# Kernel tuning notes

Measured on AMD Instinct MI355X. Metric: run time of the kernel, lower is better.

The kernel has to match this reference:

```python
import jax, jax.numpy as jnp
import numpy as np

D = 1024      # d_model
H = 16        # n_heads
HD = D // H   # head_dim = 64
B = 2
T = 2048


def setup_inputs() -> dict:
    key = jax.random.key(0)
    k0, k1, k2 = jax.random.split(key, 3)
    s = 1.0 / np.sqrt(D)
    return {
        "x": jax.random.normal(k0, (B, T, D), dtype=jnp.float32),
        "qkv_w": jax.random.normal(k1, (D, 3 * D), dtype=jnp.float32) * s,
        "qkv_b": jnp.zeros((3 * D,), dtype=jnp.float32),
        "out_w": jax.random.normal(k2, (D, D), dtype=jnp.float32) * s,
        "out_b": jnp.zeros((D,), dtype=jnp.float32),
    }


def _apply_rotary(x, rope):
    # Faithful to the torch apply_rotary: even/odd interleaved split of both
    # x and the [sin(freqs)|cos(freqs)] rope table.
    x1, x2 = x[..., ::2], x[..., 1::2]
    sin, cos = rope[..., ::2], rope[..., 1::2]
    return jnp.concatenate([x1 * cos - x2 * sin, x1 * sin + x2 * cos], axis=-1)


def reference(x, qkv_w, qkv_b, out_w, out_b):
    Bx, Tx, Dm = x.shape
    # QKV projection -> [3, B, H, T, HD]
    qkv = (x @ qkv_w + qkv_b).reshape(Bx, Tx, 3, H, HD).transpose(2, 0, 3, 1, 4)
    q, k, v = qkv[0], qkv[1], qkv[2]

    # Rotary table: rope = concat(sin(freqs), cos(freqs)) along last dim -> [T, HD]
    inv_freq = 1.0 / (10000.0 ** (jnp.arange(0, HD, 2, dtype=jnp.float32) / HD))
    t = jnp.arange(Tx, dtype=jnp.float32)
    freqs = t[:, None] * inv_freq[None, :]          # [T, HD/2]
    rope = jnp.concatenate([jnp.sin(freqs), jnp.cos(freqs)], axis=-1)  # [T, HD]

    q = _apply_rotary(q, rope)
    k = _apply_rotary(k, rope)

    scale = HD ** -0.5
    scores = jnp.einsum('bhqd,bhkd->bhqk', q, k) * scale  # [B,H,T,T]
    causal_mask = jnp.triu(jnp.ones((Tx, Tx), dtype=bool), 1)
    scores = jnp.where(causal_mask, -jnp.inf, scores)
    attn = jax.nn.softmax(scores, axis=-1)
    # dropout is identity in eval mode
    out = jnp.einsum('bhqk,bhkd->bhqd', attn, v)           # [B,H,T,HD]
    out = out.transpose(0, 2, 1, 3).reshape(Bx, Tx, Dm)    # [B,T,D]
    return out @ out_w + out_b
```

## Files before the change

### kernel.cpp

```cpp
#include <hip/hip_runtime.h>

typedef unsigned short u16;
typedef __attribute__((ext_vector_type(8))) __bf16 bf16x8;
typedef __attribute__((ext_vector_type(4))) float f32x4;

#define NB 2
#define NT 2048
#define ND 1024
#define NH 16
#define HD 64

__device__ __forceinline__ float b2f(u16 u) {
  union { float f; unsigned int i; } v; v.i = ((unsigned int)u) << 16; return v.f;
}
__device__ __forceinline__ u16 f2b(float f) {
  union { float f; unsigned int i; } v; v.f = f;
  unsigned int r = (v.i + 0x7FFFu + ((v.i >> 16) & 1u)) >> 16;
  return (u16)r;
}
__device__ __forceinline__ unsigned int cvtpk(float lo, float hi) {
  unsigned int pk;
  asm("v_cvt_pk_bf16_f32 %0, %1, %2" : "=v"(pk) : "v"(lo), "v"(hi));
  return pk;
}

__device__ __forceinline__ void gload_lds16(const u16* g, u16* lds) {
  __builtin_amdgcn_global_load_lds(
      (const __attribute__((address_space(1))) unsigned int*)(g),
      (__attribute__((address_space(3))) unsigned int*)(lds),
      16, 0, 0);
}

__device__ __forceinline__ f32x4 mfma16(bf16x8 a, bf16x8 b, f32x4 c) {
  return __builtin_amdgcn_mfma_f32_16x16x32_bf16(a, b, c, 0, 0, 0);
}

template <int N>
__device__ __forceinline__ float ror16(float x) {
  return __int_as_float(__builtin_amdgcn_update_dpp(
      __float_as_int(x), __float_as_int(x), 0x120 | N, 0xF, 0xF, true));
}
__device__ __forceinline__ float rsum16(float x) {
  x += ror16<8>(x);
  x += ror16<4>(x);
  x += ror16<2>(x);
  x += ror16<1>(x);
  return x;
}

__device__ __forceinline__ float fast_sin(float a) {
  float r = a * 0.15915494309189535f;
  r -= floorf(r);
  return __builtin_amdgcn_sinf(r);
}
__device__ __forceinline__ float fast_cos(float a) {
  float r = a * 0.15915494309189535f;
  r -= floorf(r);
  return __builtin_amdgcn_cosf(r);
}

__global__ __launch_bounds__(256) void prep_inputs(
    const float* __restrict__ x, const float* __restrict__ qkv_w,
    const float* __restrict__ out_w, u16* __restrict__ xb,
    u16* __restrict__ wqkvT, u16* __restrict__ woutT) {
  __shared__ u16 tile[32][33];
  const int blk = blockIdx.x;
  const int tid = threadIdx.x;
  if (blk < 2048) {
    int i = (blk * 256 + tid) * 8;
#pragma unroll
    for (int j = 0; j < 8; ++j) xb[i + j] = f2b(x[i + j]);
    return;
  }
  const float* in; u16* out; int N; int idx;
  if (blk < 5120) { idx = blk - 2048; in = qkv_w; out = wqkvT; N = 3072; }
  else            { idx = blk - 5120; in = out_w; out = woutT; N = 1024; }
  const int nbx = N / 32;
  const int n0 = (idx % nbx) * 32, k0 = (idx / nbx) * 32;
  const int tx = tid & 31, ty = tid >> 5;
  for (int i2 = ty; i2 < 32; i2 += 8)
    tile[i2][tx] = f2b(in[(size_t)(k0 + i2) * N + n0 + tx]);
  __syncthreads();
  for (int i2 = ty; i2 < 32; i2 += 8)
    out[(size_t)(n0 + i2) * 1024 + k0 + tx] = tile[tx][i2];
}

__global__ __launch_bounds__(256, 2) void gemm128_2ph(const u16* __restrict__ A,
                                                      const u16* __restrict__ Bt,
                                                      const float* __restrict__ bias,
                                                      float* __restrict__ C,
                                                      int M, int N, int K) {
  __shared__ alignas(16) u16 lds[2][2][8192];
  const int tid = threadIdx.x;
  const int lane = tid & 63;
  const int wave = tid >> 6;
  const int l15 = lane & 15, quad = lane >> 4;
  const int wm = (wave >> 1) * 64, wn = (wave & 1) * 64;

  const int lin = blockIdx.y * gridDim.x + blockIdx.x;
  const int xcd = lin & 7, loc = lin >> 3;
  const int row0 = (xcd * 4 + (loc >> 3)) * 128;
  const int col0 = (loc & 7) * 128;

  const int sr = tid >> 3;
  const size_t soff = (size_t)sr * K + (size_t)((tid & 7) ^ (sr & 7)) * 8;
  const u16* Ab = A + (size_t)row0 * K;
  const u16* Bb = Bt + (size_t)col0 * K;

  const int swz0 = (quad ^ (l15 & 7)) * 8;
  const int swz1 = ((4 + quad) ^ (l15 & 7)) * 8;
  const int arow = (wm + l15) * 64;
  const int brow = (wn + l15) * 64;

  f32x4 acc[4][4] = {};
  const int NTIL = K >> 6;

#define STAGE8(dst, bptr, koff)                                              \
  _Pragma("unroll") for (int p = 0; p < 4; ++p)                              \
      gload_lds16((bptr) + (koff) + soff + (size_t)p * 32 * K,               \
                  &(dst)[(p * 256 + tid) * 8]);

  STAGE8(lds[0][0], Ab, 0);
  STAGE8(lds[0][1], Bb, 0);
  asm volatile("s_waitcnt vmcnt(0)");
  __builtin_amdgcn_s_barrier();
  asm volatile("" ::: "memory");

  for (int t = 0; t < NTIL; ++t) {
    const int cur = t & 1;
    if (t + 1 < NTIL) {
      STAGE8(lds[cur ^ 1][0], Ab, (size_t)(t + 1) * 64);
      STAGE8(lds[cur ^ 1][1], Bb, (size_t)(t + 1) * 64);
    }
    bf16x8 af[4][2], bfr[4][2];
#pragma unroll
    for (int i = 0; i < 4; ++i) {
      af[i][0]  = *(const bf16x8*)&lds[cur][0][arow + i * 1024 + swz0];
      af[i][1]  = *(const bf16x8*)&lds[cur][0][arow + i * 1024 + swz1];
      bfr[i][0] = *(const bf16x8*)&lds[cur][1][brow + i * 1024 + swz0];
      bfr[i][1] = *(const bf16x8*)&lds[cur][1][brow + i * 1024 + swz1];
    }
    asm volatile("s_waitcnt lgkmcnt(0)");
    __builtin_amdgcn_sched_barrier(0);
#pragma unroll
    for (int i = 0; i < 4; ++i)
#pragma unroll
      for (int j = 0; j < 4; ++j) {
        acc[i][j] = mfma16(af[i][0], bfr[j][0], acc[i][j]);
        acc[i][j] = mfma16(af[i][1], bfr[j][1], acc[i][j]);
      }
    asm volatile("s_waitcnt vmcnt(0)");
    __builtin_amdgcn_s_barrier();
    asm volatile("" ::: "memory");
  }
#undef STAGE8

#pragma unroll
  for (int j = 0; j < 4; ++j) {
    const int c = col0 + wn + j * 16 + l15;
    const float bv = bias[c];
#pragma unroll
    for (int i = 0; i < 4; ++i) {
      const int rr0 = row0 + wm + i * 16 + quad * 4;
      f32x4 v = acc[i][j];
#pragma unroll
      for (int rr = 0; rr < 4; ++rr)
        C[(size_t)(rr0 + rr) * N + c] = v[rr] + bv;
    }
  }
}

__device__ __forceinline__ void stage2(const u16* g0, const u16* g1, u16* l,
                                       int tid) {
  gload_lds16(g0, &l[tid * 8]);
  gload_lds16(g1, &l[(512 + tid) * 8]);
}

#define AH(b, h) (&lds[((b) * 2 + (h)) * 8192])
#define BH(b, h) (&lds[32768 + ((b) * 2 + (h)) * 8192])

#define LOAD_AFX(dst, base)                                                 \
  _Pragma("unroll") for (int mm = 0; mm < 4; ++mm) {                        \
    dst[mm][0] = *(const bf16x8*)&(base)[arow + mm * 2048 + swz0];          \
    dst[mm][1] = *(const bf16x8*)&(base)[arow + mm * 2048 + swz1];          \
  }
#define LOAD_BF(base)                                                       \
  _Pragma("unroll") for (int nn = 0; nn < 2; ++nn) {                        \
    bfr[nn][0] = *(const bf16x8*)&(base)[brow + nn * 4096 + swz0];          \
    bfr[nn][1] = *(const bf16x8*)&(base)[brow + nn * 4096 + swz1];          \
  }
#define MFMA_QX(afv, MA, NQ)                                                \
  _Pragma("unroll") for (int mm = 0; mm < 4; ++mm)                          \
  _Pragma("unroll") for (int nn = 0; nn < 2; ++nn) {                        \
    acc[(MA) * 4 + mm][(NQ) * 2 + nn] =                                     \
        mfma16(afv[mm][0], bfr[nn][0], acc[(MA) * 4 + mm][(NQ) * 2 + nn]);  \
    acc[(MA) * 4 + mm][(NQ) * 2 + nn] =                                     \
        mfma16(afv[mm][1], bfr[nn][1], acc[(MA) * 4 + mm][(NQ) * 2 + nn]);  \
  }
#define PH_SYNC                                                             \
  __builtin_amdgcn_s_barrier();                                             \
  asm volatile("s_waitcnt lgkmcnt(0)");                                     \
  __builtin_amdgcn_sched_barrier(0);                                        \
  __builtin_amdgcn_s_setprio(1);
#define PH_END                                                              \
  __builtin_amdgcn_s_setprio(0);                                            \
  __builtin_amdgcn_s_barrier();                                             \
  asm volatile("" ::: "memory");

__global__ __launch_bounds__(512, 2) void gemm256_bt(const u16* __restrict__ A,
                                                     const u16* __restrict__ Bt,
                                                     const float* __restrict__ bias,
                                                     u16* __restrict__ C,
                                                     int M, int N, int K) {
  __shared__ alignas(16) u16 lds[65536];
  const int tid = threadIdx.x;
  const int lane = tid & 63;
  const int wave = tid >> 6;
  const int l15 = lane & 15, quad = lane >> 4;
  const int wm = wave >> 2, wn = wave & 3;

  const int lin = blockIdx.y * gridDim.x + blockIdx.x;
  const int xcd = lin & 7, loc = lin >> 3;
  const int row0 = ((xcd & 3) * 4 + loc / 6) * 256;
  const int col0 = ((xcd >> 2) * 6 + loc % 6) * 256;
  const int NTIL = K >> 6;

  const int sr = tid >> 3;
  const size_t soff = (size_t)sr * K + (size_t)((tid & 7) ^ (sr & 7)) * 8;
  const size_t hK = (size_t)64 * K;
  const u16* A0p = A + (size_t)row0 * K + soff;
  const u16* A1p = A0p + 2 * hK;
  const u16* B0p = Bt + (size_t)col0 * K + soff;
  const u16* B1p = B0p + 2 * hK;

  const int swz0 = (quad ^ (l15 & 7)) * 8;
  const int swz1 = ((4 + quad) ^ (l15 & 7)) * 8;
  const int arow = (wm * 16 + l15) * 64;
  const int brow = (wn * 16 + l15) * 64;

  f32x4 acc[8][4] = {};

  stage2(B0p, B0p + hK, BH(0, 0), tid);
  stage2(A1p, A1p + hK, AH(0, 1), tid);
  stage2(A0p, A0p + hK, AH(0, 0), tid);
  stage2(B1p, B1p + hK, BH(0, 1), tid);
  {
    int tp = (NTIL > 1) ? 1 : 0;
    stage2(B0p + tp * 64, B0p + tp * 64 + hK, BH(1, 0), tid);
    stage2(A1p + tp * 64, A1p + tp * 64 + hK, AH(1, 1), tid);
  }
  asm volatile("s_waitcnt vmcnt(4)");
  __builtin_amdgcn_s_barrier();
  asm volatile("" ::: "memory");

  bf16x8 afA[4][2], afB[4][2], bfr[2][2];
#pragma unroll 2
  for (int t = 0; t < NTIL; ++t) {
    const int cur = t & 1, nxt = cur ^ 1;
    const int o1 = ((t + 1 < NTIL) ? t + 1 : NTIL - 1) * 64;
    const int o2 = ((t + 2 < NTIL) ? t + 2 : NTIL - 1) * 64;
    u16* Ac0 = AH(cur, 0);
    u16* Ac1 = AH(cur, 1);
    u16* Bc0 = BH(cur, 0);
    u16* Bc1 = BH(cur, 1);

    LOAD_AFX(afA, Ac0);
    LOAD_BF(Bc0);
    stage2(A0p + o1, A0p + o1 + hK, AH(nxt, 0), tid);
    PH_SYNC; MFMA_QX(afA, 0, 0); PH_END;

    LOAD_AFX(afB, Ac1);
    stage2(B1p + o1, B1p + o1 + hK, BH(nxt, 1), tid);
    PH_SYNC; MFMA_QX(afB, 1, 0); PH_END;

    LOAD_BF(Bc1);
    stage2(B0p + o2, B0p + o2 + hK, Bc0, tid);
    PH_SYNC; MFMA_QX(afB, 1, 1); PH_END;

    stage2(A1p + o2, A1p + o2 + hK, Ac1, tid);
    __builtin_amdgcn_s_barrier();
    __builtin_amdgcn_sched_barrier(0);
    __builtin_amdgcn_s_setprio(1);
    MFMA_QX(afA, 0, 1);
    __builtin_amdgcn_s_setprio(0);
    asm volatile("s_waitcnt vmcnt(4)");
    __builtin_amdgcn_s_barrier();
    asm volatile("" ::: "memory");
  }
  asm volatile("s_waitcnt vmcnt(0)");

#pragma unroll
  for (int ni = 0; ni < 4; ++ni) {
    const int col = col0 + (ni >> 1) * 128 + (ni & 1) * 64 + wn * 16 + l15;
    const float bv = bias[col];
#pragma unroll
    for (int mi = 0; mi < 8; ++mi) {
      const int r0 = row0 + (mi >> 2) * 128 + (mi & 3) * 32 + wm * 16 + quad * 4;
      f32x4 v = acc[mi][ni];
#pragma unroll
      for (int rr = 0; rr < 4; ++rr)
        C[(size_t)(r0 + rr) * N + col] = f2b(v[rr] + bv);
    }
  }
}

__global__ __launch_bounds__(256) void prep_frag(const u16* __restrict__ qkv,
                                                 u16* __restrict__ qsw,
                                                 u16* __restrict__ ksw,
                                                 u16* __restrict__ vsw) {
  __shared__ u16 tq[32 * 72];
  __shared__ u16 tk[32 * 72];
  __shared__ u16 tv[32 * 72];
  const int bh = blockIdx.y;
  const int b = bh >> 4, h = bh & 15;
  const int t0 = blockIdx.x * 32;
  const int tid = threadIdx.x;

  {
    int row = tid >> 3, col = (tid & 7) * 8;
    const u16* src = &qkv[(size_t)(b * NT + t0 + row) * 3072 + h * HD + col];
    *(bf16x8*)&tq[row * 72 + col] = *(const bf16x8*)src;
    *(bf16x8*)&tk[row * 72 + col] = *(const bf16x8*)(src + ND);
    *(bf16x8*)&tv[row * 72 + col] = *(const bf16x8*)(src + 2 * ND);
  }
  __syncthreads();

  {
    const int isK = tid >> 7;
    const int chunk = (tid >> 4) & 7;
    const int tl = tid & 15;
    const int ks = chunk >> 2, quad = chunk & 3;
    const u16* tile = isK ? tk : tq;
    u16* dst = isK ? ksw : qsw;
    const float scale = isK ? 1.0f : 0.125f;
    const float LOG1E4 = 9.210340371976184f;

#pragma unroll
    for (int rbloc = 0; rbloc < 2; ++rbloc) {
      const int row = rbloc * 16 + tl;
      const float tf = (float)(t0 + row);
      union { u16 s[8]; unsigned int u[4]; bf16x8 v; } o;
      float ovv[8];
#pragma unroll
      for (int e = 0; e < 8; ++e) {
        int c = ks * 32 + quad * 8 + e;
        int j = c & 31;
        int c1 = 2 * j, c2 = 2 * j + 1;
        float inv1 = __expf(-((float)(c1 & 31)) * (1.0f / 32.0f) * LOG1E4);
        float inv2 = __expf(-((float)(c2 & 31)) * (1.0f / 32.0f) * LOG1E4);
        float a1 = tf * inv1, a2 = tf * inv2;
        float sA = (c1 < 32) ? fast_sin(a1) : fast_cos(a1);
        float cA = (c2 < 32) ? fast_sin(a2) : fast_cos(a2);
        float x1 = b2f(tile[row * 72 + c1]), x2 = b2f(tile[row * 72 + c2]);
        float ov = (c < 32) ? (x1 * cA - x2 * sA) : (x1 * sA + x2 * cA);
        ovv[e] = ov * scale;
      }
#pragma unroll
      for (int p2 = 0; p2 < 4; ++p2)
        o.u[p2] = cvtpk(ovv[2 * p2], ovv[2 * p2 + 1]);
      size_t addr =
          ((((size_t)bh * 128 + (t0 >> 4) + rbloc) * 2 + ks) * 64 + quad * 16 + tl) * 8;
      *(bf16x8*)&dst[addr] = o.v;
    }
  }

  {
    const int ni = tid >> 6, lane = tid & 63;
    const int quad = lane >> 4, l15 = lane & 15;
    union { u16 s[8]; bf16x8 v; } o;
#pragma unroll
    for (int e = 0; e < 8; ++e) {
      int p = quad * 8 + e;
      int krow = (p >> 1) + ((p & 1) << 4);
      o.s[e] = tv[krow * 72 + ni * 16 + l15];
    }
    *(bf16x8*)&vsw[(((size_t)bh * 64 + (t0 >> 5)) * 4 + ni) * 512 + lane * 8] = o.v;
  }
}

__global__ __launch_bounds__(128, 2) void flash_kernel(const u16* __restrict__ qsw,
                                                       const u16* __restrict__ ksw,
                                                       const u16* __restrict__ vsw,
                                                       u16* __restrict__ attn) {
  __shared__ alignas(16) u16 Ps[2 * 5120];
  float* const Of = (float*)&Ps[5120];
  float* const Ll = (float*)&Ps[9216];

  const int tid = threadIdx.x;
  const int w = tid >> 6;
  const int lane = tid & 63;
  const int l15 = lane & 15, quad = lane >> 4;
  const int linear = (int)blockIdx.x;
  const int bh = linear & 31;
  const int qt = 63 - (linear >> 5);
  const int r0 = qt * 32;
  u16* Psw = &Ps[w * 5120];

  bf16x8 aq[2][2];
#pragma unroll
  for (int mi = 0; mi < 2; ++mi)
#pragma unroll
    for (int ks = 0; ks < 2; ++ks)
      aq[mi][ks] = *(const bf16x8*)&qsw[
          ((((size_t)bh * 128 + qt * 2 + mi) * 2 + ks) * 64 + lane) * 8];

  f32x4 oacc[2][4] = {};
  float lst[8] = {0.f, 0.f, 0.f, 0.f, 0.f, 0.f, 0.f, 0.f};

  const int ktmax = qt >> 2;
  for (int kt = w; kt <= ktmax; kt += 2) {
    bf16x8 kf[2][8];
#pragma unroll
    for (int ks = 0; ks < 2; ++ks)
#pragma unroll
      for (int ni = 0; ni < 8; ++ni)
        kf[ks][ni] = *(const bf16x8*)&ksw[
            ((((size_t)bh * 128 + kt * 8 + ni) * 2 + ks) * 64 + lane) * 8];

    f32x4 sacc[2][8] = {};
#pragma unroll
    for (int ks = 0; ks < 2; ++ks)
#pragma unroll
      for (int ni = 0; ni < 8; ++ni) {
        sacc[0][ni] = mfma16(aq[0][ks], kf[ks][ni], sacc[0][ni]);
        sacc[1][ni] = mfma16(aq[1][ks], kf[ks][ni], sacc[1][ni]);
      }

    bf16x8 vf[4][4];
#pragma unroll
    for (int ks = 0; ks < 4; ++ks)
#pragma unroll
      for (int ni = 0; ni < 4; ++ni)
        vf[ks][ni] = *(const bf16x8*)&vsw[
            (((size_t)bh * 64 + kt * 4 + ks) * 4 + ni) * 512 + lane * 8];

    const bool diag = (kt == ktmax);
    const int k0 = kt * 128;
#pragma unroll
    for (int mi = 0; mi < 2; ++mi)
#pragma unroll
      for (int r = 0; r < 4; ++r) {
        const int prow = mi * 16 + quad * 4 + r;
        float sv[8];
#pragma unroll
        for (int ni = 0; ni < 8; ++ni) sv[ni] = sacc[mi][ni][r];
        if (diag) {
#pragma unroll
          for (int ni = 0; ni < 8; ++ni)
            if (k0 + ni * 16 + l15 > r0 + prow) sv[ni] = -__builtin_inff();
        }
        float rs = 0.f;
#pragma unroll
        for (int ni = 0; ni < 8; ++ni) {
          float p = __expf(sv[ni]);
          sv[ni] = p;
          rs += p;
        }
        lst[mi * 4 + r] += rsum16(rs);
#pragma unroll
        for (int ni = 0; ni < 8; ni += 2) {
          unsigned int pk = cvtpk(sv[ni], sv[ni + 1]);
          *(unsigned int*)&Psw[(ni >> 1) * 1280 + prow * 40 + 2 * l15] = pk;
        }
      }

    asm volatile("" ::: "memory");

#pragma unroll
    for (int ks = 0; ks < 4; ++ks) {
      bf16x8 ap0 = *(const bf16x8*)&Psw[ks * 1280 + l15 * 40 + quad * 8];
      bf16x8 ap1 = *(const bf16x8*)&Psw[ks * 1280 + (16 + l15) * 40 + quad * 8];
#pragma unroll
      for (int ni = 0; ni < 4; ++ni) {
        oacc[0][ni] = mfma16(ap0, vf[ks][ni], oacc[0][ni]);
        oacc[1][ni] = mfma16(ap1, vf[ks][ni], oacc[1][ni]);
      }
    }
  }

  if (w == 1) {
#pragma unroll
    for (int mi = 0; mi < 2; ++mi)
#pragma unroll
      for (int r = 0; r < 4; ++r) {
        const int row = mi * 16 + quad * 4 + r;
        if (l15 == 0) Ll[row] = lst[mi * 4 + r];
#pragma unroll
        for (int ni = 0; ni < 4; ++ni)
          Of[row * 64 + ni * 16 + l15] = oacc[mi][ni][r];
      }
  }
  __syncthreads();
  if (w == 0) {
    const int b = bh >> 4, h = bh & 15;
#pragma unroll
    for (int mi = 0; mi < 2; ++mi)
#pragma unroll
      for (int r = 0; r < 4; ++r) {
        const int row = mi * 16 + quad * 4 + r;
        const float rl = 1.0f / (lst[mi * 4 + r] + Ll[row]);
        const int trow = r0 + row;
#pragma unroll
        for (int ni = 0; ni < 4; ++ni) {
          float o = oacc[mi][ni][r] + Of[row * 64 + ni * 16 + l15];
          attn[((size_t)b * NT + trow) * ND + h * HD + ni * 16 + l15] = f2b(o * rl);
        }
      }
  }
}

extern "C" void kernel_launch(void* const* d_in, const int* in_sizes, int n_in,
                              void* d_out, int out_size, void* d_ws, size_t ws_size,
                              hipStream_t stream) {
  const float* x = (const float*)d_in[0];
  const float* qkv_w = (const float*)d_in[1];
  const float* qkv_b = (const float*)d_in[2];
  const float* out_w = (const float*)d_in[3];
  const float* out_b = (const float*)d_in[4];
  float* out = (float*)d_out;

  u16* ws = (u16*)d_ws;
  u16* xb    = ws;
  u16* wqkvT = xb + (size_t)4096 * 1024;
  u16* woutT = wqkvT + 3072 * 1024;
  u16* qkv   = woutT + 1024 * 1024;
  u16* qsw   = qkv + (size_t)4096 * 3072;
  u16* ksw   = qsw + (size_t)32 * 2048 * 64;
  u16* vsw   = ksw + (size_t)32 * 2048 * 64;
  u16* attn  = vsw + (size_t)32 * 2048 * 64;

  prep_inputs<<<dim3(6144), 256, 0, stream>>>(x, qkv_w, out_w, xb, wqkvT, woutT);

  gemm256_bt<<<dim3(3 * ND / 256, NB * NT / 256), 512, 0, stream>>>(
      xb, wqkvT, qkv_b, qkv, NB * NT, 3 * ND, ND);

  prep_frag<<<dim3(NT / 32, NB * NH), 256, 0, stream>>>(qkv, qsw, ksw, vsw);

  flash_kernel<<<dim3(2048), 128, 0, stream>>>(qsw, ksw, vsw, attn);

  gemm128_2ph<<<dim3(ND / 128, NB * NT / 128), 256, 0, stream>>>(
      attn, woutT, out_b, out, NB * NT, ND, ND);
}
```

Measured before the change: 179.7 us.

## Fuse rotary and fragment-swizzle prep into QKV GEMM epilogue via LDS

The QKV GEMM now stages its 256x256 output tile in LDS with an XOR swizzle. From there it applies rotary embedding and Q scaling and writes the attention-ready Q/K/V fragment layouts directly. This removes the separate prep_frag kernel and the round-trip of the full qkv intermediate through global memory. In exchange the GEMM epilogue gains serial loops with sin/cos work and extra barriers, and it runs at the GEMM's lower occupancy.

```diff
diff --git a/kernel.cpp b/kernel.cpp
--- a/kernel.cpp
+++ b/kernel.cpp
@@ -176,6 +176,11 @@
   gload_lds16(g1, &l[(512 + tid) * 8]);
 }
 
+__device__ __forceinline__ u16* tsw(u16* base, int row, int col) {
+  int byte = row * 512 + ((col * 2) ^ ((row & 15) << 4));
+  return (u16*)((char*)base + byte);
+}
+
 #define AH(b, h) (&lds[((b) * 2 + (h)) * 8192])
 #define BH(b, h) (&lds[32768 + ((b) * 2 + (h)) * 8192])
 
@@ -207,11 +212,13 @@
   __builtin_amdgcn_s_barrier();                                             \
   asm volatile("" ::: "memory");
 
-__global__ __launch_bounds__(512, 2) void gemm256_bt(const u16* __restrict__ A,
-                                                     const u16* __restrict__ Bt,
-                                                     const float* __restrict__ bias,
-                                                     u16* __restrict__ C,
-                                                     int M, int N, int K) {
+__global__ __launch_bounds__(512, 2) void gemm256_qkv(const u16* __restrict__ A,
+                                                      const u16* __restrict__ Bt,
+                                                      const float* __restrict__ bias,
+                                                      u16* __restrict__ qsw,
+                                                      u16* __restrict__ ksw,
+                                                      u16* __restrict__ vsw,
+                                                      int K) {
   __shared__ alignas(16) u16 lds[65536];
   const int tid = threadIdx.x;
   const int lane = tid & 63;
@@ -288,93 +295,94 @@
     asm volatile("" ::: "memory");
   }
   asm volatile("s_waitcnt vmcnt(0)");
+  __syncthreads();
 
 #pragma unroll
   for (int ni = 0; ni < 4; ++ni) {
-    const int col = col0 + (ni >> 1) * 128 + (ni & 1) * 64 + wn * 16 + l15;
-    const float bv = bias[col];
+    const int col_in = (ni >> 1) * 128 + (ni & 1) * 64 + wn * 16 + l15;
+    const float bv = bias[col0 + col_in];
 #pragma unroll
     for (int mi = 0; mi < 8; ++mi) {
-      const int r0 = row0 + (mi >> 2) * 128 + (mi & 3) * 32 + wm * 16 + quad * 4;
+      const int r_in0 = (mi >> 2) * 128 + (mi & 3) * 32 + wm * 16 + quad * 4;
       f32x4 v = acc[mi][ni];
 #pragma unroll
       for (int rr = 0; rr < 4; ++rr)
-        C[(size_t)(r0 + rr) * N + col] = f2b(v[rr] + bv);
-    }
-  }
-}
-
-__global__ __launch_bounds__(256) void prep_frag(const u16* __restrict__ qkv,
-                                                 u16* __restrict__ qsw,
-                                                 u16* __restrict__ ksw,
-                                                 u16* __restrict__ vsw) {
-  __shared__ u16 tq[32 * 72];
-  __shared__ u16 tk[32 * 72];
-  __shared__ u16 tv[32 * 72];
-  const int bh = blockIdx.y;
-  const int b = bh >> 4, h = bh & 15;
-  const int t0 = blockIdx.x * 32;
-  const int tid = threadIdx.x;
-
-  {
-    int row = tid >> 3, col = (tid & 7) * 8;
-    const u16* src = &qkv[(size_t)(b * NT + t0 + row) * 3072 + h * HD + col];
-    *(bf16x8*)&tq[row * 72 + col] = *(const bf16x8*)src;
-    *(bf16x8*)&tk[row * 72 + col] = *(const bf16x8*)(src + ND);
-    *(bf16x8*)&tv[row * 72 + col] = *(const bf16x8*)(src + 2 * ND);
+        *tsw(lds, r_in0 + rr, col_in) = f2b(v[rr] + bv);
+    }
   }
   __syncthreads();
 
-  {
-    const int isK = tid >> 7;
+  const int tt = col0 >> 10;
+  const int h0 = (col0 & 1023) >> 6;
+  const int bb = row0 >> 11;
+  const int tb0 = row0 & 2047;
+
+  if (tt < 2) {
+    u16* dst = (tt == 0) ? qsw : ksw;
+    const float scale = (tt == 0) ? 0.125f : 1.0f;
+    const float LOG1E4 = 9.210340371976184f;
+    const int hh = tid >> 7;
     const int chunk = (tid >> 4) & 7;
     const int tl = tid & 15;
-    const int ks = chunk >> 2, quad = chunk & 3;
-    const u16* tile = isK ? tk : tq;
-    u16* dst = isK ? ksw : qsw;
-    const float scale = isK ? 1.0f : 0.125f;
-    const float LOG1E4 = 9.210340371976184f;
-
-#pragma unroll
-    for (int rbloc = 0; rbloc < 2; ++rbloc) {
-      const int row = rbloc * 16 + tl;
-      const float tf = (float)(t0 + row);
-      union { u16 s[8]; unsigned int u[4]; bf16x8 v; } o;
-      float ovv[8];
+    const int ks = chunk >> 2, qd = chunk & 3;
+    const int bh = bb * 16 + h0 + hh;
+    float inv1a[8], inv2a[8];
+    int cc[8], c1a[8], c2a[8];
+#pragma unroll
+    for (int e = 0; e < 8; ++e) {
+      int c = ks * 32 + qd * 8 + e;
+      int j = c & 31;
+      cc[e] = c; c1a[e] = 2 * j; c2a[e] = 2 * j + 1;
+      inv1a[e] = __expf(-((float)(c1a[e] & 31)) * (1.0f / 32.0f) * LOG1E4);
+      inv2a[e] = __expf(-((float)(c2a[e] & 31)) * (1.0f / 32.0f) * LOG1E4);
+    }
+    for (int tb = 0; tb < 8; ++tb) {
+      const int tbt = tb0 + tb * 32;
+#pragma unroll
+      for (int rbloc = 0; rbloc < 2; ++rbloc) {
+        const int rrow = tb * 32 + rbloc * 16 + tl;
+        const float tf = (float)(tbt + rbloc * 16 + tl);
+        union { u16 s[8]; unsigned int u[4]; bf16x8 v; } o;
+        float ovv[8];
+#pragma unroll
+        for (int e = 0; e < 8; ++e) {
+          float a1 = tf * inv1a[e], a2 = tf * inv2a[e];
+          float sA = (c1a[e] < 32) ? fast_sin(a1) : fast_cos(a1);
+          float cA = (c2a[e] < 32) ? fast_sin(a2) : fast_cos(a2);
+          float x1 = b2f(*tsw(lds, rrow, hh * 64 + c1a[e]));
+          float x2 = b2f(*tsw(lds, rrow, hh * 64 + c2a[e]));
+          float ov = (cc[e] < 32) ? (x1 * cA - x2 * sA) : (x1 * sA + x2 * cA);
+          ovv[e] = ov * scale;
+        }
+#pragma unroll
+        for (int p2 = 0; p2 < 4; ++p2)
+          o.u[p2] = cvtpk(ovv[2 * p2], ovv[2 * p2 + 1]);
+        size_t addr =
+            ((((size_t)bh * 128 + (tbt >> 4) + rbloc) * 2 + ks) * 64 +
+             qd * 16 + tl) * 8;
+        *(bf16x8*)&dst[addr] = o.v;
+      }
+    }
+  } else {
+    const int u = tid >> 8;
+    const int utid = tid & 255;
+    const int ni = utid >> 6, lane2 = utid & 63;
+    const int qd = lane2 >> 4, l15b = lane2 & 15;
+    for (int it = 0; it < 16; ++it) {
+      const int unit = it * 2 + u;
+      const int hh = unit >> 3, tb = unit & 7;
+      const int bh = bb * 16 + h0 + hh;
+      const int tbt = tb0 + tb * 32;
+      union { u16 s[8]; bf16x8 v; } o;
 #pragma unroll
       for (int e = 0; e < 8; ++e) {
-        int c = ks * 32 + quad * 8 + e;
-        int j = c & 31;
-        int c1 = 2 * j, c2 = 2 * j + 1;
-        float inv1 = __expf(-((float)(c1 & 31)) * (1.0f / 32.0f) * LOG1E4);
-        float inv2 = __expf(-((float)(c2 & 31)) * (1.0f / 32.0f) * LOG1E4);
-        float a1 = tf * inv1, a2 = tf * inv2;
-        float sA = (c1 < 32) ? fast_sin(a1) : fast_cos(a1);
-        float cA = (c2 < 32) ? fast_sin(a2) : fast_cos(a2);
-        float x1 = b2f(tile[row * 72 + c1]), x2 = b2f(tile[row * 72 + c2]);
-        float ov = (c < 32) ? (x1 * cA - x2 * sA) : (x1 * sA + x2 * cA);
-        ovv[e] = ov * scale;
-      }
-#pragma unroll
-      for (int p2 = 0; p2 < 4; ++p2)
-        o.u[p2] = cvtpk(ovv[2 * p2], ovv[2 * p2 + 1]);
-      size_t addr =
-          ((((size_t)bh * 128 + (t0 >> 4) + rbloc) * 2 + ks) * 64 + quad * 16 + tl) * 8;
-      *(bf16x8*)&dst[addr] = o.v;
-    }
-  }
-
-  {
-    const int ni = tid >> 6, lane = tid & 63;
-    const int quad = lane >> 4, l15 = lane & 15;
-    union { u16 s[8]; bf16x8 v; } o;
-#pragma unroll
-    for (int e = 0; e < 8; ++e) {
-      int p = quad * 8 + e;
-      int krow = (p >> 1) + ((p & 1) << 4);
-      o.s[e] = tv[krow * 72 + ni * 16 + l15];
-    }
-    *(bf16x8*)&vsw[(((size_t)bh * 64 + (t0 >> 5)) * 4 + ni) * 512 + lane * 8] = o.v;
+        int p = qd * 8 + e;
+        int krow = (p >> 1) + ((p & 1) << 4);
+        o.s[e] = *tsw(lds, tb * 32 + krow, hh * 64 + ni * 16 + l15b);
+      }
+      *(bf16x8*)&vsw[(((size_t)bh * 64 + (tbt >> 5)) * 4 + ni) * 512 +
+                     lane2 * 8] = o.v;
+    }
   }
 }
 
@@ -523,18 +531,15 @@
   u16* xb    = ws;
   u16* wqkvT = xb + (size_t)4096 * 1024;
   u16* woutT = wqkvT + 3072 * 1024;
-  u16* qkv   = woutT + 1024 * 1024;
-  u16* qsw   = qkv + (size_t)4096 * 3072;
+  u16* qsw   = woutT + 1024 * 1024;
   u16* ksw   = qsw + (size_t)32 * 2048 * 64;
   u16* vsw   = ksw + (size_t)32 * 2048 * 64;
   u16* attn  = vsw + (size_t)32 * 2048 * 64;
 
   prep_inputs<<<dim3(6144), 256, 0, stream>>>(x, qkv_w, out_w, xb, wqkvT, woutT);
 
-  gemm256_bt<<<dim3(3 * ND / 256, NB * NT / 256), 512, 0, stream>>>(
-      xb, wqkvT, qkv_b, qkv, NB * NT, 3 * ND, ND);
-
-  prep_frag<<<dim3(NT / 32, NB * NH), 256, 0, stream>>>(qkv, qsw, ksw, vsw);
+  gemm256_qkv<<<dim3(12, 16), 512, 0, stream>>>(
+      xb, wqkvT, qkv_b, qsw, ksw, vsw, ND);
 
   flash_kernel<<<dim3(2048), 128, 0, stream>>>(qsw, ksw, vsw, attn);
 
```

Result: no change. 179.8 us (+0.1%).
